# Kernel optimization log

Hardware: AMD Instinct MI355X
Metric: run time of the kernel (lower is better)

The kernel has to match this reference:

```python
import jax, jax.numpy as jnp
import numpy as np

B, S, D = 16, 2048, 400
HEADS, HEAD_SIZE = 4, 100
SCALE = 1.0 / np.float32(100.0 ** 0.5)


def setup_inputs() -> dict:
    key = jax.random.key(0)
    ks = jax.random.split(key, 8)
    return {
        "x": jax.random.normal(ks[0], (B, S, D), jnp.float32),
        "attn_kernel": jax.random.normal(ks[1], (3, D, HEAD_SIZE), jnp.float32) * 0.05,
        "attn_dense": jax.random.normal(ks[2], (D, HEADS * HEAD_SIZE), jnp.float32) * 0.05,
        "d1_w": jax.random.normal(ks[3], (400, 400), jnp.float32) * 0.05,
        "d1_b": jnp.zeros((400,), jnp.float32),
        "fc1_w": jax.random.normal(ks[4], (800, 512), jnp.float32) * 0.05,
        "fc1_b": jnp.zeros((512,), jnp.float32),
        "fc2_w": jax.random.normal(ks[5], (512, 256), jnp.float32) * 0.05,
        "fc2_b": jnp.zeros((256,), jnp.float32),
    }


def reference(x, attn_kernel, attn_dense, d1_w, d1_b, fc1_w, fc1_b, fc2_w, fc2_b):
    # Multi-head attention. NOTE: the original loops `heads` times over the SAME
    # shared kernel, so all 4 head outputs are identical; compute once, tile.
    WQ = jnp.einsum('bsd,dh->bsh', x, attn_kernel[0])  # [B,S,100]
    WK = jnp.einsum('bsd,dh->bsh', x, attn_kernel[1])
    WV = jnp.einsum('bsd,dh->bsh', x, attn_kernel[2])
    scores = jnp.einsum('bqh,bkh->bqk', WQ, WK) * SCALE  # [B,S,S]
    probs = jax.nn.softmax(scores, axis=-1)
    V = jnp.einsum('bqk,bkh->bqh', probs, WV)  # [B,S,100]
    out = jnp.tile(V, (1, 1, HEADS))  # concat of identical heads -> [B,S,400]
    out = jnp.einsum('bsd,de->bse', out, attn_dense)  # [B,S,400]
    # Dropout layers are identity at inference.
    h = jax.nn.relu(jnp.einsum('bsd,de->bse', out, d1_w) + d1_b)  # [B,S,400]
    pooled = jnp.concatenate([jnp.max(h, axis=1), jnp.mean(h, axis=1)], axis=-1)  # [B,800]
    h = jax.nn.relu(pooled @ fc1_w + fc1_b)  # [B,512]
    h = jax.nn.relu(h @ fc2_w + fc2_b)  # [B,256]
    return h
```

## Files before the change

kernel.cpp:

```cpp
#include <hip/hip_runtime.h>

typedef __attribute__((ext_vector_type(8))) _Float16 f16x8;
typedef __attribute__((ext_vector_type(4))) float f4v;
typedef __attribute__((ext_vector_type(8))) unsigned short us8;
typedef __attribute__((ext_vector_type(4))) unsigned short us4;
typedef unsigned short u16;

__device__ __forceinline__ u16 h2b(_Float16 h) { return __builtin_bit_cast(u16, h); }
__device__ __forceinline__ float b2f(u16 b) {
    return (float)__builtin_bit_cast(_Float16, b);
}

#define BAR() do { asm volatile("s_waitcnt lgkmcnt(0)" ::: "memory"); \
                   __builtin_amdgcn_s_barrier(); } while (0)

__global__ void k_prep(const float* __restrict__ ak, u16* __restrict__ wsp,
                       const float* __restrict__ ad, const float* __restrict__ d1w,
                       float* __restrict__ w2p) {
    const int bx = blockIdx.x, tid = threadIdx.x;
    if (bx < 624) {
        int i = bx * 256 + tid;
        if (i >= 159744) return;
        int k = i & 31, n = (i >> 5) & 127;
        int xx = i >> 12;
        int ks = xx % 13, m = xx / 13;
        int gk = ks * 32 + k;
        float v = (n < 100 && gk < 400) ? ak[m * 40000 + gk * 100 + n] : 0.f;
        _Float16 hb = (_Float16)v;
        _Float16 lb = (_Float16)(v - (float)hb);
        long base = (long)xx * 8192;
        int pos = n * 32 + ((((k >> 3) ^ (n & 3)) << 3) | (k & 7));
        wsp[base + pos] = h2b(hb);
        wsp[base + 4096 + pos] = h2b(lb);
    } else {
        int j2 = bx - 624;
        int es = j2 / 200;
        int i = (j2 % 200) * 256 + tid;
        if (i >= 51200) return;
        int d = i / 400, j = i % 400;
        float acc = 0.f;
        if (d < 100) {
            const float* a0 = ad + d * 400 + es * 100;
            const float* wr = d1w + (es * 100) * 400 + j;
            #pragma unroll 4
            for (int e = 0; e < 100; ++e) {
                float av = a0[e] + a0[40000 + e] + a0[80000 + e] + a0[120000 + e];
                acc += av * wr[e * 400];
            }
        }
        w2p[es * 51200 + i] = acc;
    }
}

__global__ void k_w2r(const float* __restrict__ w2p, u16* __restrict__ w2f) {
    int i = blockIdx.x * 256 + threadIdx.x;
    if (i >= 51200) return;
    float acc = w2p[i] + w2p[51200 + i] + w2p[102400 + i] + w2p[153600 + i];
    int d = i / 400, j = i % 400;
    int idx = ((j >> 4) * 4 + (d >> 5)) * 512 + (((d >> 3) & 3) * 16 + (j & 15)) * 8 + (d & 7);
    w2f[idx] = h2b((_Float16)acc);
}

__global__ __launch_bounds__(512) void k_gemm_qkv(
    const float* __restrict__ x, const u16* __restrict__ wsp,
    u16* __restrict__ QH, u16* __restrict__ KH, u16* __restrict__ VT) {
    __shared__ __align__(16) u16 smem[32768];

    const int tid = threadIdx.x;
    const int rowblk = blockIdx.x;
    const long row0 = (long)rowblk * 64;
    const int w = tid >> 6, l = tid & 63, g = l >> 4, c15 = l & 15;
    const int wm = w & 3, wn = w >> 2;
    const int sr = (tid & 255) >> 2, skc = tid & 3;
    const bool xload = tid < 256;

    f4v aQ[4], aK[4], aV[4];
    #pragma unroll
    for (int j = 0; j < 4; ++j) {
        aQ[j] = (f4v){0.f, 0.f, 0.f, 0.f};
        aK[j] = (f4v){0.f, 0.f, 0.f, 0.f};
        aV[j] = (f4v){0.f, 0.f, 0.f, 0.f};
    }

    const u16* wq  = wsp;
    const u16* wkh = wsp + 106496;
    const u16* wv  = wsp + 212992;

    float4 xr0, xr1;
    us8 wr[3];
    const int xpos = sr * 32 + ((skc * 8) ^ ((sr & 3) << 3));

    {
        if (xload) {
            const float* xp = x + (row0 + sr) * 400 + skc * 8;
            xr0 = *(const float4*)xp;
            xr1 = *(const float4*)(xp + 4);
        }
        wr[0] = *(const us8*)&wq [(long)tid * 8];
        wr[1] = *(const us8*)&wkh[(long)tid * 8];
        wr[2] = *(const us8*)&wv [(long)tid * 8];
        if (xload) {
            float va[8] = {xr0.x, xr0.y, xr0.z, xr0.w, xr1.x, xr1.y, xr1.z, xr1.w};
            us8 hi8, lo8;
            #pragma unroll
            for (int j = 0; j < 8; ++j) {
                _Float16 h = (_Float16)va[j];
                hi8[j] = h2b(h);
                lo8[j] = h2b((_Float16)(va[j] - (float)h));
            }
            *(us8*)&smem[xpos] = hi8;
            *(us8*)&smem[2048 + xpos] = lo8;
        }
        *(us8*)&smem[4096  + tid * 8] = wr[0];
        *(us8*)&smem[8192  + tid * 8] = wr[1];
        *(us8*)&smem[12288 + tid * 8] = wr[2];
        if (xload) {
            const float* xp1 = x + (row0 + sr) * 400 + 32 + skc * 8;
            xr0 = *(const float4*)xp1;
            xr1 = *(const float4*)(xp1 + 4);
        }
        wr[0] = *(const us8*)&wq [8192 + (long)tid * 8];
        wr[1] = *(const us8*)&wkh[8192 + (long)tid * 8];
        wr[2] = *(const us8*)&wv [8192 + (long)tid * 8];
    }

    for (int ks = 0; ks < 13; ++ks) {
        BAR();
        u16* cb = smem + (ks & 1) * 16384;
        u16* sb = smem + ((ks & 1) ^ 1) * 16384;
        if (ks + 1 < 13) {
            if (xload) {
                float va[8] = {xr0.x, xr0.y, xr0.z, xr0.w, xr1.x, xr1.y, xr1.z, xr1.w};
                us8 hi8, lo8;
                #pragma unroll
                for (int j = 0; j < 8; ++j) {
                    _Float16 h = (_Float16)va[j];
                    hi8[j] = h2b(h);
                    lo8[j] = h2b((_Float16)(va[j] - (float)h));
                }
                *(us8*)&sb[xpos] = hi8;
                *(us8*)&sb[2048 + xpos] = lo8;
            }
            *(us8*)&sb[4096  + tid * 8] = wr[0];
            *(us8*)&sb[8192  + tid * 8] = wr[1];
            *(us8*)&sb[12288 + tid * 8] = wr[2];
            if (ks + 2 < 13) {
                if (xload) {
                    if ((ks + 2) * 32 + skc * 8 < 400) {
                        const float* xp = x + (row0 + sr) * 400 + (ks + 2) * 32 + skc * 8;
                        xr0 = *(const float4*)xp;
                        xr1 = *(const float4*)(xp + 4);
                    } else {
                        xr0 = make_float4(0.f, 0.f, 0.f, 0.f);
                        xr1 = make_float4(0.f, 0.f, 0.f, 0.f);
                    }
                }
                long wo = (long)(ks + 2) * 8192 + (long)tid * 8;
                wr[0] = *(const us8*)&wq [wo];
                wr[1] = *(const us8*)&wkh[wo];
                wr[2] = *(const us8*)&wv [wo];
            }
        }
        const int arow = wm * 16 + c15;
        const int axo = arow * 32 + ((g * 8) ^ ((arow & 3) << 3));
        f16x8 ah = *(const f16x8*)&cb[axo];
        f16x8 al = *(const f16x8*)&cb[2048 + axo];
        __builtin_amdgcn_s_setprio(1);
        #pragma unroll
        for (int j = 0; j < 4; ++j) {
            int brow = (wn * 4 + j) * 16 + c15;
            int boff = brow * 32 + ((g * 8) ^ ((brow & 3) << 3));
            f16x8 qb = *(const f16x8*)&cb[4096 + boff];
            aQ[j] = __builtin_amdgcn_mfma_f32_16x16x32_f16(ah, qb, aQ[j], 0, 0, 0);
            aQ[j] = __builtin_amdgcn_mfma_f32_16x16x32_f16(al, qb, aQ[j], 0, 0, 0);
            f16x8 kh = *(const f16x8*)&cb[8192 + boff];
            aK[j] = __builtin_amdgcn_mfma_f32_16x16x32_f16(ah, kh, aK[j], 0, 0, 0);
            aK[j] = __builtin_amdgcn_mfma_f32_16x16x32_f16(al, kh, aK[j], 0, 0, 0);
            f16x8 vb = *(const f16x8*)&cb[12288 + boff];
            aV[j] = __builtin_amdgcn_mfma_f32_16x16x32_f16(ah, vb, aV[j], 0, 0, 0);
            aV[j] = __builtin_amdgcn_mfma_f32_16x16x32_f16(al, vb, aV[j], 0, 0, 0);
        }
        __builtin_amdgcn_s_setprio(0);
    }
    BAR();
    u16* epi = smem;

    {
        const float qs = 0.14426950408889634f;
        #pragma unroll
        for (int j = 0; j < 4; ++j) {
            #pragma unroll
            for (int r = 0; r < 4; ++r) {
                int row = wm * 16 + 4 * g + r, col = (wn * 4 + j) * 16 + c15;
                epi[row * 128 + (col ^ ((row & 7) << 3))] =
                    h2b((_Float16)(aQ[j][r] * qs));
            }
        }
        __syncthreads();
        #pragma unroll
        for (int r = 0; r < 2; ++r) {
            int u = tid + r * 512;
            int row = u >> 4, c = u & 15;
            *(us8*)&QH[(row0 + row) * 128 + c * 8] =
                *(const us8*)&epi[row * 128 + ((c * 8) ^ ((row & 7) << 3))];
        }
        __syncthreads();
    }
    {
        #pragma unroll
        for (int j = 0; j < 4; ++j) {
            #pragma unroll
            for (int r = 0; r < 4; ++r) {
                int row = wm * 16 + 4 * g + r, col = (wn * 4 + j) * 16 + c15;
                epi[row * 128 + (col ^ ((row & 7) << 3))] = h2b((_Float16)aK[j][r]);
            }
        }
        __syncthreads();
        u16* dst = KH + (long)rowblk * 8192;
        #pragma unroll
        for (int r = 0; r < 2; ++r) {
            int u = tid + r * 512;
            *(us8*)&dst[(long)u * 8] = *(const us8*)&epi[u * 8];
        }
        __syncthreads();
    }
    {
        const int q0 = wm * 16 + 4 * g;
        #pragma unroll
        for (int j = 0; j < 4; ++j) {
            int d = (wn * 4 + j) * 16 + c15;
            if (d < 112) {
                us4 v4;
                #pragma unroll
                for (int r = 0; r < 4; ++r) v4[r] = h2b((_Float16)aV[j][r]);
                *(us4*)&epi[d * 64 + (q0 ^ ((d & 7) << 3))] = v4;
            }
        }
        __syncthreads();
        #pragma unroll
        for (int r = 0; r < 2; ++r) {
            int u = tid + r * 512;
            if (u < 896)
                *(us8*)&VT[(long)rowblk * 7168 + (long)u * 8] =
                    *(const us8*)&epi[u * 8];
        }
    }
}

__global__ __launch_bounds__(512) void k_flash(
    const u16* __restrict__ Qg, const u16* __restrict__ Kg,
    const u16* __restrict__ Vg, u16* __restrict__ VOI,
    float* __restrict__ ML) {
    __shared__ __align__(16) char KS[2][16384];
    __shared__ __align__(16) char VS[2][14336];
    __shared__ __align__(16) char PS[8][2048];

    const int tid = threadIdx.x;
    const int w = tid >> 6, l = tid & 63, g = l >> 4, c15 = l & 15;
    const int b = blockIdx.y, qt = blockIdx.x, half = blockIdx.z;
    const int t0 = half * 16;

    const u16* qp = Qg + ((long)b * 2048 + qt * 128 + w * 16 + c15) * 128;
    f16x8 qh[4];
    #pragma unroll
    for (int ks = 0; ks < 4; ++ks) qh[ks] = *(const f16x8*)(qp + ks * 32 + g * 8);

    f4v O[7];
    #pragma unroll
    for (int i = 0; i < 7; ++i) O[i] = (f4v){0.f, 0.f, 0.f, 0.f};
    float lrow = 0.f;

    const char* Kb = (const char*)(Kg + (long)b * 32 * 8192);
    const char* Vb = (const char*)(Vg + (long)b * 32 * 7168);
    char* Pw = PS[w];

    us8 kreg[2], vreg[2];
    #pragma unroll
    for (int r = 0; r < 2; ++r) {
        int u = tid + r * 512;
        kreg[r] = *(const us8*)(Kb + (long)t0 * 16384 + (long)u * 16);
        if (u < 896) vreg[r] = *(const us8*)(Vb + (long)t0 * 14336 + (long)u * 16);
    }
    #pragma unroll
    for (int r = 0; r < 2; ++r) {
        int u = tid + r * 512;
        *(us8*)(KS[0] + u * 16) = kreg[r];
        if (u < 896) *(us8*)(VS[0] + u * 16) = vreg[r];
    }
    #pragma unroll
    for (int r = 0; r < 2; ++r) {
        int u = tid + r * 512;
        kreg[r] = *(const us8*)(Kb + (long)(t0 + 1) * 16384 + (long)u * 16);
        if (u < 896) vreg[r] = *(const us8*)(Vb + (long)(t0 + 1) * 14336 + (long)u * 16);
    }

    for (int t = t0; t < t0 + 16; ++t) {
        const int cur = (t - t0) & 1;
        BAR();
        if (t + 1 < t0 + 16) {
            #pragma unroll
            for (int r = 0; r < 2; ++r) {
                int u = tid + r * 512;
                *(us8*)(KS[cur ^ 1] + u * 16) = kreg[r];
                if (u < 896) *(us8*)(VS[cur ^ 1] + u * 16) = vreg[r];
            }
            if (t + 2 < t0 + 16) {
                #pragma unroll
                for (int r = 0; r < 2; ++r) {
                    int u = tid + r * 512;
                    kreg[r] = *(const us8*)(Kb + (long)(t + 2) * 16384 + (long)u * 16);
                    if (u < 896)
                        vreg[r] = *(const us8*)(Vb + (long)(t + 2) * 14336 + (long)u * 16);
                }
            }
        }
        const char* Kc = KS[cur];
        const char* Vc = VS[cur];

        f4v s[4];
        #pragma unroll
        for (int nt = 0; nt < 4; ++nt) s[nt] = (f4v){0.f, 0.f, 0.f, 0.f};
        __builtin_amdgcn_s_setprio(1);
        #pragma unroll
        for (int ks = 0; ks < 4; ++ks) {
            #pragma unroll
            for (int nt = 0; nt < 4; ++nt) {
                int key = nt * 16 + c15;
                f16x8 kf = *(const f16x8*)(Kc + key * 256 +
                                           ((ks * 64 + g * 16) ^ ((key & 7) << 4)));
                s[nt] = __builtin_amdgcn_mfma_f32_16x16x32_f16(kf, qh[ks], s[nt], 0, 0, 0);
            }
        }
        __builtin_amdgcn_s_setprio(0);

        float sum = 0.f;
        #pragma unroll
        for (int nt = 0; nt < 4; ++nt) {
            #pragma unroll
            for (int r = 0; r < 4; ++r) {
                float p = exp2f(s[nt][r]);
                s[nt][r] = p;
                sum += p;
            }
        }
        sum += __shfl_xor(sum, 16);
        sum += __shfl_xor(sum, 32);
        lrow += sum;

        #pragma unroll
        for (int nt = 0; nt < 4; ++nt) {
            uint2 pw2;
            pw2.x = __builtin_bit_cast(unsigned int,
                        __builtin_amdgcn_cvt_pkrtz(s[nt][0], s[nt][1]));
            pw2.y = __builtin_bit_cast(unsigned int,
                        __builtin_amdgcn_cvt_pkrtz(s[nt][2], s[nt][3]));
            *(uint2*)(Pw + c15 * 128 + ((32 * nt + 8 * g) ^ ((c15 & 7) << 4))) = pw2;
        }
        __builtin_amdgcn_s_setprio(1);
        #pragma unroll
        for (int k0 = 0; k0 < 2; ++k0) {
            f16x8 pa = *(const f16x8*)(Pw + c15 * 128 +
                                       ((k0 * 64 + g * 16) ^ ((c15 & 7) << 4)));
            #pragma unroll
            for (int dt = 0; dt < 7; ++dt) {
                int d = dt * 16 + c15;
                f16x8 vf = *(const f16x8*)(Vc + d * 128 +
                                           ((k0 * 64 + g * 16) ^ ((d & 7) << 4)));
                O[dt] = __builtin_amdgcn_mfma_f32_16x16x32_f16(pa, vf, O[dt], 0, 0, 0);
            }
        }
        __builtin_amdgcn_s_setprio(0);
    }

    if (g == 0) {
        ((float*)Pw)[c15] = lrow;
        ML[half * 32768 + b * 2048 + qt * 128 + w * 16 + c15] = lrow;
    }
    float linv[4];
    #pragma unroll
    for (int r = 0; r < 4; ++r) linv[r] = 1.f / ((float*)Pw)[4 * g + r];
    u16* vout = VOI + ((long)(half * 16 + b) * 2048 + qt * 128 + w * 16) * 112;
    #pragma unroll
    for (int r = 0; r < 4; ++r) {
        int row = 4 * g + r;
        #pragma unroll
        for (int dt = 0; dt < 7; ++dt)
            vout[row * 112 + dt * 16 + c15] =
                h2b((_Float16)(O[dt][r] * linv[r]));
    }
}

__global__ __launch_bounds__(256) void k_hpool(
    const u16* __restrict__ VOI, const float* __restrict__ ML,
    const u16* __restrict__ W2F, const float* __restrict__ d1b,
    float* __restrict__ pmax, float* __restrict__ psum) {
    __shared__ __align__(16) u16 A[8192];
    __shared__ float redM[4][400], redS[4][400];
    __shared__ float wgt[64][2];
    const int tid = threadIdx.x;
    const int w = tid >> 6, l = tid & 63, g = l >> 4, c15 = l & 15;
    const int b = blockIdx.y, rt = blockIdx.x;

    if (tid < 64) {
        float a = ML[b * 2048 + rt * 64 + tid];
        float c = ML[32768 + b * 2048 + rt * 64 + tid];
        float inv = 1.f / (a + c);
        wgt[tid][0] = a * inv;
        wgt[tid][1] = c * inv;
    }
    if (tid < 128) {
        int r = tid >> 1, c = 14 + (tid & 1);
        us8 z = {0, 0, 0, 0, 0, 0, 0, 0};
        *(us8*)&A[r * 128 + ((c * 8) ^ ((r & 7) << 3))] = z;
    }
    __syncthreads();

    const u16* s1 = VOI + ((long)b * 2048 + rt * 64) * 112;
    const u16* s2 = VOI + ((long)(16 + b) * 2048 + rt * 64) * 112;
    #pragma unroll
    for (int r = 0; r < 4; ++r) {
        int u = tid + r * 256;
        if (u < 896) {
            int row = u / 14, c = u % 14;
            us8 p1 = *(const us8*)&s1[row * 112 + c * 8];
            us8 p2 = *(const us8*)&s2[row * 112 + c * 8];
            float w1 = wgt[row][0], w2 = wgt[row][1];
            us8 o;
            #pragma unroll
            for (int j = 0; j < 8; ++j)
                o[j] = h2b((_Float16)(w1 * b2f(p1[j]) + w2 * b2f(p2[j])));
            *(us8*)&A[row * 128 + ((c * 8) ^ ((row & 7) << 3))] = o;
        }
    }
    __syncthreads();

    const int arow = w * 16 + c15;
    f16x8 af[4];
    #pragma unroll
    for (int ks = 0; ks < 4; ++ks)
        af[ks] = *(const f16x8*)&A[arow * 128 + ((ks * 32 + g * 8) ^ ((arow & 7) << 3))];

    for (int nt = 0; nt < 25; ++nt) {
        f4v acc = (f4v){0.f, 0.f, 0.f, 0.f};
        #pragma unroll
        for (int ks = 0; ks < 4; ++ks) {
            f16x8 bf = *(const f16x8*)&W2F[(nt * 4 + ks) * 512 + l * 8];
            acc = __builtin_amdgcn_mfma_f32_16x16x32_f16(af[ks], bf, acc, 0, 0, 0);
        }
        float bias = d1b[nt * 16 + c15];
        float mx4 = -1e30f, sm4 = 0.f;
        #pragma unroll
        for (int r = 0; r < 4; ++r) {
            float h = fmaxf(acc[r] + bias, 0.f);
            mx4 = fmaxf(mx4, h);
            sm4 += h;
        }
        mx4 = fmaxf(mx4, __shfl_xor(mx4, 16));
        mx4 = fmaxf(mx4, __shfl_xor(mx4, 32));
        sm4 += __shfl_xor(sm4, 16);
        sm4 += __shfl_xor(sm4, 32);
        if (g == 0) {
            redM[w][nt * 16 + c15] = mx4;
            redS[w][nt * 16 + c15] = sm4;
        }
    }
    __syncthreads();
    for (int j = tid; j < 400; j += 256) {
        float mx = fmaxf(fmaxf(redM[0][j], redM[1][j]), fmaxf(redM[2][j], redM[3][j]));
        float sm = redS[0][j] + redS[1][j] + redS[2][j] + redS[3][j];
        pmax[((long)b * 32 + rt) * 400 + j] = mx;
        psum[((long)b * 32 + rt) * 400 + j] = sm;
    }
}

__global__ __launch_bounds__(256) void k_pred(
    const float* __restrict__ pmax, const float* __restrict__ psum,
    float* __restrict__ pooled) {
    __shared__ float rm[16][17], rs[16][17];
    const int b = blockIdx.x, jt = blockIdx.y, tid = threadIdx.x;
    const int jo = tid & 15, ts = tid >> 4;
    const int j = jt * 16 + jo;
    float mx = -1e30f, sm = 0.f;
    for (int t = ts; t < 32; t += 16) {
        mx = fmaxf(mx, pmax[((long)b * 32 + t) * 400 + j]);
        sm += psum[((long)b * 32 + t) * 400 + j];
    }
    rm[ts][jo] = mx; rs[ts][jo] = sm;
    __syncthreads();
    if (tid < 16) {
        float m2 = rm[0][tid], s2 = rs[0][tid];
        #pragma unroll
        for (int t = 1; t < 16; ++t) { m2 = fmaxf(m2, rm[t][tid]); s2 += rs[t][tid]; }
        pooled[b * 800 + jt * 16 + tid] = m2;
        pooled[b * 800 + 400 + jt * 16 + tid] = s2 * (1.f / 2048.f);
    }
}

__global__ __launch_bounds__(256) void k_fc1(
    const float* __restrict__ pooled, const float* __restrict__ w,
    const float* __restrict__ bias, float* __restrict__ out) {
    __shared__ float pl[800];
    __shared__ float red[16][17];
    const int b = blockIdx.x, jt = blockIdx.y, tid = threadIdx.x;
    const int jo = tid & 15, ks = tid >> 4;
    const int j = jt * 16 + jo;
    for (int i = tid; i < 800; i += 256) pl[i] = pooled[b * 800 + i];
    __syncthreads();
    float acc = 0.f;
    #pragma unroll 5
    for (int kk = 0; kk < 50; ++kk) {
        int k = ks * 50 + kk;
        acc += pl[k] * w[k * 512 + j];
    }
    red[ks][jo] = acc;
    __syncthreads();
    if (tid < 16) {
        float s = red[0][tid];
        #pragma unroll
        for (int t = 1; t < 16; ++t) s += red[t][tid];
        out[b * 512 + jt * 16 + tid] = fmaxf(s + bias[jt * 16 + tid], 0.f);
    }
}

__global__ __launch_bounds__(256) void k_fc2(
    const float* __restrict__ h, const float* __restrict__ w,
    const float* __restrict__ bias, float* __restrict__ out) {
    __shared__ float hl[512];
    __shared__ float red[16][17];
    const int b = blockIdx.x, jt = blockIdx.y, tid = threadIdx.x;
    const int jo = tid & 15, ks = tid >> 4;
    const int j = jt * 16 + jo;
    for (int i = tid; i < 512; i += 256) hl[i] = h[b * 512 + i];
    __syncthreads();
    float acc = 0.f;
    #pragma unroll 4
    for (int kk = 0; kk < 32; ++kk) {
        int k = ks * 32 + kk;
        acc += hl[k] * w[k * 256 + j];
    }
    red[ks][jo] = acc;
    __syncthreads();
    if (tid < 16) {
        float s = red[0][tid];
        #pragma unroll
        for (int t = 1; t < 16; ++t) s += red[t][tid];
        out[b * 256 + jt * 16 + tid] = fmaxf(s + bias[jt * 16 + tid], 0.f);
    }
}

extern "C" void kernel_launch(void* const* d_in, const int* in_sizes, int n_in,
                              void* d_out, int out_size, void* d_ws, size_t ws_size,
                              hipStream_t stream) {
    const float* x          = (const float*)d_in[0];
    const float* attn_kernel= (const float*)d_in[1];
    const float* attn_dense = (const float*)d_in[2];
    const float* d1_w       = (const float*)d_in[3];
    const float* d1_b       = (const float*)d_in[4];
    const float* fc1_w      = (const float*)d_in[5];
    const float* fc1_b      = (const float*)d_in[6];
    const float* fc2_w      = (const float*)d_in[7];
    const float* fc2_b      = (const float*)d_in[8];
    float* out = (float*)d_out;
    char*  wsb = (char*)d_ws;

    u16*    QH   = (u16*)(wsb);
    u16*    KH   = (u16*)(wsb + 8388608);
    u16*    VT   = (u16*)(wsb + 16777216);
    u16*    VOI  = (u16*)(wsb + 24117248);
    u16*    WSP  = (u16*)(wsb + 38797312);
    u16*    W2F  = (u16*)(wsb + 39436288);
    float*  PMAX = (float*)(wsb + 39538688);
    float*  PSUM = (float*)(wsb + 40357888);
    float*  ML   = (float*)(wsb + 41177088);
    float*  W2P  = (float*)(wsb + 41439232);
    float*  POOL = (float*)(wsb + 42258432);
    float*  FC1  = (float*)(wsb + 42309632);

    k_prep<<<1424, 256, 0, stream>>>(attn_kernel, WSP, attn_dense, d1_w, W2P);
    k_w2r <<<200, 256, 0, stream>>>(W2P, W2F);
    k_gemm_qkv<<<512, 512, 0, stream>>>(x, WSP, QH, KH, VT);
    k_flash<<<dim3(16, 16, 2), 512, 0, stream>>>(QH, KH, VT, VOI, ML);
    k_hpool<<<dim3(32, 16), 256, 0, stream>>>(VOI, ML, W2F, d1_b, PMAX, PSUM);
    k_pred<<<dim3(16, 25), 256, 0, stream>>>(PMAX, PSUM, POOL);
    k_fc1 <<<dim3(16, 32), 256, 0, stream>>>(POOL, fc1_w, fc1_b, FC1);
    k_fc2 <<<dim3(16, 16), 256, 0, stream>>>(FC1, fc2_w, fc2_b, out);
}
```

Before: 129.7 us.

## Split flash keys across wave pairs so each K fragment feeds two query tiles

The flash kernel now gives each wave 32 query rows and half of each 64-key tile, instead of 16 rows over all keys. Each K fragment read from LDS feeds two MFMAs and each V fragment serves two P tiles, which halves per-wave LDS fragment traffic. Partial O accumulators and row sums from the two key-halves are merged through shared memory at the end, at the cost of more registers and an extra exchange with barriers. Separately, the weight-fold prep splits the reduction over 8 chunks of 50 instead of 4 of 100 for more parallelism, with k_w2r summing 8 partials and the workspace offsets moved to fit.

```diff
diff --git a/kernel.cpp b/kernel.cpp
--- a/kernel.cpp
+++ b/kernel.cpp
@@ -40,10 +40,10 @@
         int d = i / 400, j = i % 400;
         float acc = 0.f;
         if (d < 100) {
-            const float* a0 = ad + d * 400 + es * 100;
-            const float* wr = d1w + (es * 100) * 400 + j;
-            #pragma unroll 4
-            for (int e = 0; e < 100; ++e) {
+            const float* a0 = ad + d * 400 + es * 50;
+            const float* wr = d1w + (es * 50) * 400 + j;
+            #pragma unroll 5
+            for (int e = 0; e < 50; ++e) {
                 float av = a0[e] + a0[40000 + e] + a0[80000 + e] + a0[120000 + e];
                 acc += av * wr[e * 400];
             }
@@ -55,7 +55,9 @@
 __global__ void k_w2r(const float* __restrict__ w2p, u16* __restrict__ w2f) {
     int i = blockIdx.x * 256 + threadIdx.x;
     if (i >= 51200) return;
-    float acc = w2p[i] + w2p[51200 + i] + w2p[102400 + i] + w2p[153600 + i];
+    float acc = 0.f;
+    #pragma unroll
+    for (int s = 0; s < 8; ++s) acc += w2p[s * 51200 + i];
     int d = i / 400, j = i % 400;
     int idx = ((j >> 4) * 4 + (d >> 5)) * 512 + (((d >> 3) & 3) * 16 + (j & 15)) * 8 + (d & 7);
     w2f[idx] = h2b((_Float16)acc);
@@ -251,28 +253,32 @@
     const u16* __restrict__ Qg, const u16* __restrict__ Kg,
     const u16* __restrict__ Vg, u16* __restrict__ VOI,
     float* __restrict__ ML) {
-    __shared__ __align__(16) char KS[2][16384];
-    __shared__ __align__(16) char VS[2][14336];
-    __shared__ __align__(16) char PS[8][2048];
+    __shared__ __align__(16) char smem[77824];
 
     const int tid = threadIdx.x;
-    const int w = tid >> 6, l = tid & 63, g = l >> 4, c15 = l & 15;
+    const int w = tid >> 6, l = tid & 63, g = (l >> 4) & 3, c15 = l & 15;
+    const int qg = w & 3, kh = w >> 2;
     const int b = blockIdx.y, qt = blockIdx.x, half = blockIdx.z;
     const int t0 = half * 16;
 
-    const u16* qp = Qg + ((long)b * 2048 + qt * 128 + w * 16 + c15) * 128;
-    f16x8 qh[4];
-    #pragma unroll
-    for (int ks = 0; ks < 4; ++ks) qh[ks] = *(const f16x8*)(qp + ks * 32 + g * 8);
-
-    f4v O[7];
-    #pragma unroll
-    for (int i = 0; i < 7; ++i) O[i] = (f4v){0.f, 0.f, 0.f, 0.f};
-    float lrow = 0.f;
+    const u16* qp = Qg + ((long)b * 2048 + qt * 128 + qg * 32 + c15) * 128;
+    f16x8 qh[2][4];
+    #pragma unroll
+    for (int h = 0; h < 2; ++h)
+        #pragma unroll
+        for (int ks = 0; ks < 4; ++ks)
+            qh[h][ks] = *(const f16x8*)(qp + h * 2048 + ks * 32 + g * 8);
+
+    f4v O[2][7];
+    #pragma unroll
+    for (int h = 0; h < 2; ++h)
+        #pragma unroll
+        for (int i = 0; i < 7; ++i) O[h][i] = (f4v){0.f, 0.f, 0.f, 0.f};
+    float lrow[2] = {0.f, 0.f};
 
     const char* Kb = (const char*)(Kg + (long)b * 32 * 8192);
     const char* Vb = (const char*)(Vg + (long)b * 32 * 7168);
-    char* Pw = PS[w];
+    char* Pw = smem + 61440 + w * 2048;
 
     us8 kreg[2], vreg[2];
     #pragma unroll
@@ -284,8 +290,8 @@
     #pragma unroll
     for (int r = 0; r < 2; ++r) {
         int u = tid + r * 512;
-        *(us8*)(KS[0] + u * 16) = kreg[r];
-        if (u < 896) *(us8*)(VS[0] + u * 16) = vreg[r];
+        *(us8*)(smem + u * 16) = kreg[r];
+        if (u < 896) *(us8*)(smem + 32768 + u * 16) = vreg[r];
     }
     #pragma unroll
     for (int r = 0; r < 2; ++r) {
@@ -301,8 +307,9 @@
             #pragma unroll
             for (int r = 0; r < 2; ++r) {
                 int u = tid + r * 512;
-                *(us8*)(KS[cur ^ 1] + u * 16) = kreg[r];
-                if (u < 896) *(us8*)(VS[cur ^ 1] + u * 16) = vreg[r];
+                *(us8*)(smem + (cur ^ 1) * 16384 + u * 16) = kreg[r];
+                if (u < 896)
+                    *(us8*)(smem + 32768 + (cur ^ 1) * 14336 + u * 16) = vreg[r];
             }
             if (t + 2 < t0 + 16) {
                 #pragma unroll
@@ -314,79 +321,116 @@
                 }
             }
         }
-        const char* Kc = KS[cur];
-        const char* Vc = VS[cur];
-
-        f4v s[4];
-        #pragma unroll
-        for (int nt = 0; nt < 4; ++nt) s[nt] = (f4v){0.f, 0.f, 0.f, 0.f};
+        const char* Kc = smem + cur * 16384;
+        const char* Vc = smem + 32768 + cur * 14336;
+
+        f4v s[2][2];
+        #pragma unroll
+        for (int h = 0; h < 2; ++h)
+            #pragma unroll
+            for (int nt = 0; nt < 2; ++nt) s[h][nt] = (f4v){0.f, 0.f, 0.f, 0.f};
         __builtin_amdgcn_s_setprio(1);
         #pragma unroll
         for (int ks = 0; ks < 4; ++ks) {
             #pragma unroll
-            for (int nt = 0; nt < 4; ++nt) {
-                int key = nt * 16 + c15;
+            for (int nt = 0; nt < 2; ++nt) {
+                int key = kh * 32 + nt * 16 + c15;
                 f16x8 kf = *(const f16x8*)(Kc + key * 256 +
                                            ((ks * 64 + g * 16) ^ ((key & 7) << 4)));
-                s[nt] = __builtin_amdgcn_mfma_f32_16x16x32_f16(kf, qh[ks], s[nt], 0, 0, 0);
+                s[0][nt] = __builtin_amdgcn_mfma_f32_16x16x32_f16(kf, qh[0][ks], s[0][nt], 0, 0, 0);
+                s[1][nt] = __builtin_amdgcn_mfma_f32_16x16x32_f16(kf, qh[1][ks], s[1][nt], 0, 0, 0);
             }
         }
         __builtin_amdgcn_s_setprio(0);
 
-        float sum = 0.f;
-        #pragma unroll
-        for (int nt = 0; nt < 4; ++nt) {
+        #pragma unroll
+        for (int h = 0; h < 2; ++h) {
+            float sum = 0.f;
+            #pragma unroll
+            for (int nt = 0; nt < 2; ++nt) {
+                #pragma unroll
+                for (int r = 0; r < 4; ++r) {
+                    float p = exp2f(s[h][nt][r]);
+                    s[h][nt][r] = p;
+                    sum += p;
+                }
+            }
+            sum += __shfl_xor(sum, 16);
+            sum += __shfl_xor(sum, 32);
+            lrow[h] += sum;
+        }
+
+        #pragma unroll
+        for (int h = 0; h < 2; ++h) {
+            #pragma unroll
+            for (int nt = 0; nt < 2; ++nt) {
+                uint2 pp;
+                pp.x = __builtin_bit_cast(unsigned int,
+                            __builtin_amdgcn_cvt_pkrtz(s[h][nt][0], s[h][nt][1]));
+                pp.y = __builtin_bit_cast(unsigned int,
+                            __builtin_amdgcn_cvt_pkrtz(s[h][nt][2], s[h][nt][3]));
+                *(uint2*)(Pw + (h * 16 + c15) * 64 +
+                          ((nt * 32 + g * 8) ^ ((c15 & 3) << 4))) = pp;
+            }
+        }
+        __builtin_amdgcn_s_setprio(1);
+        f16x8 pa0 = *(const f16x8*)(Pw + c15 * 64 + ((g * 16) ^ ((c15 & 3) << 4)));
+        f16x8 pa1 = *(const f16x8*)(Pw + (16 + c15) * 64 + ((g * 16) ^ ((c15 & 3) << 4)));
+        #pragma unroll
+        for (int dt = 0; dt < 7; ++dt) {
+            int d = dt * 16 + c15;
+            f16x8 vf = *(const f16x8*)(Vc + d * 128 +
+                                       ((kh * 64 + g * 16) ^ ((d & 7) << 4)));
+            O[0][dt] = __builtin_amdgcn_mfma_f32_16x16x32_f16(pa0, vf, O[0][dt], 0, 0, 0);
+            O[1][dt] = __builtin_amdgcn_mfma_f32_16x16x32_f16(pa1, vf, O[1][dt], 0, 0, 0);
+        }
+        __builtin_amdgcn_s_setprio(0);
+    }
+
+    float* PSm = (float*)Pw;
+    if (g == 0) { PSm[c15] = lrow[0]; PSm[16 + c15] = lrow[1]; }
+    BAR();
+    if (kh == 1) {
+        char* ex = smem + qg * 14336;
+        #pragma unroll
+        for (int h = 0; h < 2; ++h)
+            #pragma unroll
+            for (int dt = 0; dt < 7; ++dt)
+                *(f4v*)(ex + ((h * 7 + dt) * 64 + l) * 16) = O[h][dt];
+    }
+    BAR();
+    if (kh == 0) {
+        const char* ex = smem + qg * 14336;
+        #pragma unroll
+        for (int h = 0; h < 2; ++h)
+            #pragma unroll
+            for (int dt = 0; dt < 7; ++dt)
+                O[h][dt] += *(const f4v*)(ex + ((h * 7 + dt) * 64 + l) * 16);
+        const float* PSp = (const float*)(smem + 61440 + (w + 4) * 2048);
+        float linv[2][4];
+        #pragma unroll
+        for (int h = 0; h < 2; ++h)
             #pragma unroll
             for (int r = 0; r < 4; ++r) {
-                float p = exp2f(s[nt][r]);
-                s[nt][r] = p;
-                sum += p;
-            }
-        }
-        sum += __shfl_xor(sum, 16);
-        sum += __shfl_xor(sum, 32);
-        lrow += sum;
-
-        #pragma unroll
-        for (int nt = 0; nt < 4; ++nt) {
-            uint2 pw2;
-            pw2.x = __builtin_bit_cast(unsigned int,
-                        __builtin_amdgcn_cvt_pkrtz(s[nt][0], s[nt][1]));
-            pw2.y = __builtin_bit_cast(unsigned int,
-                        __builtin_amdgcn_cvt_pkrtz(s[nt][2], s[nt][3]));
-            *(uint2*)(Pw + c15 * 128 + ((32 * nt + 8 * g) ^ ((c15 & 7) << 4))) = pw2;
-        }
-        __builtin_amdgcn_s_setprio(1);
-        #pragma unroll
-        for (int k0 = 0; k0 < 2; ++k0) {
-            f16x8 pa = *(const f16x8*)(Pw + c15 * 128 +
-                                       ((k0 * 64 + g * 16) ^ ((c15 & 7) << 4)));
-            #pragma unroll
-            for (int dt = 0; dt < 7; ++dt) {
-                int d = dt * 16 + c15;
-                f16x8 vf = *(const f16x8*)(Vc + d * 128 +
-                                           ((k0 * 64 + g * 16) ^ ((d & 7) << 4)));
-                O[dt] = __builtin_amdgcn_mfma_f32_16x16x32_f16(pa, vf, O[dt], 0, 0, 0);
-            }
-        }
-        __builtin_amdgcn_s_setprio(0);
-    }
-
-    if (g == 0) {
-        ((float*)Pw)[c15] = lrow;
-        ML[half * 32768 + b * 2048 + qt * 128 + w * 16 + c15] = lrow;
-    }
-    float linv[4];
-    #pragma unroll
-    for (int r = 0; r < 4; ++r) linv[r] = 1.f / ((float*)Pw)[4 * g + r];
-    u16* vout = VOI + ((long)(half * 16 + b) * 2048 + qt * 128 + w * 16) * 112;
-    #pragma unroll
-    for (int r = 0; r < 4; ++r) {
-        int row = 4 * g + r;
-        #pragma unroll
-        for (int dt = 0; dt < 7; ++dt)
-            vout[row * 112 + dt * 16 + c15] =
-                h2b((_Float16)(O[dt][r] * linv[r]));
+                int q = h * 16 + 4 * g + r;
+                linv[h][r] = 1.f / (PSm[q] + PSp[q]);
+            }
+        if (l < 32) {
+            long mb = (long)half * 32768 + b * 2048 + qt * 128 + qg * 32;
+            ML[mb + l] = PSm[l] + PSp[l];
+        }
+        u16* vout = VOI + ((long)(half * 16 + b) * 2048 + qt * 128 + qg * 32) * 112;
+        #pragma unroll
+        for (int h = 0; h < 2; ++h) {
+            #pragma unroll
+            for (int r = 0; r < 4; ++r) {
+                int row = h * 16 + 4 * g + r;
+                #pragma unroll
+                for (int dt = 0; dt < 7; ++dt)
+                    vout[row * 112 + dt * 16 + c15] =
+                        h2b((_Float16)(O[h][dt][r] * linv[h][r]));
+            }
+        }
     }
 }
 
@@ -573,10 +617,10 @@
     float*  PSUM = (float*)(wsb + 40357888);
     float*  ML   = (float*)(wsb + 41177088);
     float*  W2P  = (float*)(wsb + 41439232);
-    float*  POOL = (float*)(wsb + 42258432);
-    float*  FC1  = (float*)(wsb + 42309632);
-
-    k_prep<<<1424, 256, 0, stream>>>(attn_kernel, WSP, attn_dense, d1_w, W2P);
+    float*  POOL = (float*)(wsb + 43077632);
+    float*  FC1  = (float*)(wsb + 43128832);
+
+    k_prep<<<2224, 256, 0, stream>>>(attn_kernel, WSP, attn_dense, d1_w, W2P);
     k_w2r <<<200, 256, 0, stream>>>(W2P, W2F);
     k_gemm_qkv<<<512, 512, 0, stream>>>(x, WSP, QH, KH, VT);
     k_flash<<<dim3(16, 16, 2), 512, 0, stream>>>(QH, KH, VT, VOI, ML);
```

After: 140.8 us. +8.6%, slower.
